# Kernel optimization log

Measured on AMD Instinct MI355X. Metric: run time of the kernel, lower is better.

Reference implementation:

```python
import jax, jax.numpy as jnp
import numpy as np

N, E = 10000, 160000
HID, EDIM = 256, 128
EPS = 1e-5


def _layernorm(x, g, b):
    mu = jnp.mean(x, axis=-1, keepdims=True)
    var = jnp.mean(jnp.square(x - mu), axis=-1, keepdims=True)
    return (x - mu) * jax.lax.rsqrt(var + EPS) * g + b


def setup_inputs() -> dict:
    key = jax.random.key(0)
    ks = jax.random.split(key, 12)
    cat_dim = 2 * HID + EDIM  # 640

    def lin(k, fan_in, fan_out):
        kw, kb = jax.random.split(k)
        lim = 1.0 / np.sqrt(fan_in)
        W = jax.random.uniform(kw, (fan_in, fan_out), jnp.float32, -lim, lim)
        b = jax.random.uniform(kb, (fan_out,), jnp.float32, -lim, lim)
        return W, b

    We1, be1 = lin(ks[0], cat_dim, EDIM)
    We2, be2 = lin(ks[1], EDIM, EDIM)
    Wv1, bv1 = lin(ks[2], cat_dim, HID)
    Wv2, bv2 = lin(ks[3], HID, HID)

    return {
        "h": jax.random.normal(ks[4], (N, HID), jnp.float32),
        "e": jax.random.normal(ks[5], (E, EDIM), jnp.float32),
        "edge_index": jax.random.randint(ks[6], (2, E), 0, N, jnp.int64),
        "We1": We1, "be1": be1, "We2": We2, "be2": be2,
        "Wv1": Wv1, "bv1": bv1, "Wv2": Wv2, "bv2": bv2,
        "ne_g": jnp.ones((EDIM,), jnp.float32), "ne_b": jnp.zeros((EDIM,), jnp.float32),
        "nv_g": jnp.ones((HID,), jnp.float32), "nv_b": jnp.zeros((HID,), jnp.float32),
    }


def reference(h, e, edge_index, We1, be1, We2, be2, Wv1, bv1, Wv2, bv2,
              ne_g, ne_b, nv_g, nv_b):
    # Eval mode: dropout and edge_drop are identity.
    src, dst = edge_index[0], edge_index[1]
    h_src = h[src]  # [E, HID] gather
    h_dst = h[dst]  # [E, HID] gather

    # Edge update: phi_e(concat) -> residual + LayerNorm
    xe = jnp.concatenate([h_src, h_dst, e], axis=-1)  # [E, 2H+ED]
    e_msg = jax.nn.gelu(xe @ We1 + be1, approximate=False) @ We2 + be2
    e_new = _layernorm(e + e_msg, ne_g, ne_b)

    # Node update: phi_v(concat with updated e) -> scatter_mean -> residual + LN
    xv = jnp.concatenate([h_src, h_dst, e_new], axis=-1)
    m = jax.nn.gelu(xv @ Wv1 + bv1, approximate=False) @ Wv2 + bv2  # [E, HID]
    agg = jax.ops.segment_sum(m, dst, num_segments=h.shape[0])
    counts = jax.ops.segment_sum(jnp.ones((m.shape[0], 1), m.dtype), dst,
                                 num_segments=h.shape[0])
    agg = agg / jnp.maximum(counts, 1.0)
    h_new = _layernorm(h + agg, nv_g, nv_b)
    return (h_new, e_new)
```

## Files before the change

kernel.cpp:

```cpp
#include <hip/hip_runtime.h>
#include <hip/hip_bf16.h>

#define NNODE 10000
#define NEDGE 160000
#define HIDD  256
#define ED    128
#define CAT   640

typedef short bf8 __attribute__((ext_vector_type(8)));
typedef short bf4 __attribute__((ext_vector_type(4)));
typedef float f4  __attribute__((ext_vector_type(4)));
typedef unsigned int u32;

__device__ __forceinline__ float bf2f(ushort u) {
    return __uint_as_float(((unsigned)u) << 16);
}
__device__ __forceinline__ ushort f2bf(float f) {
    unsigned u = __float_as_uint(f);
    return (ushort)((u + 0x7fffu + ((u >> 16) & 1u)) >> 16);
}
__device__ __forceinline__ float gelu_fast(float x) {
    float x2 = x * x;
    float u = 0.7978845608028654f * x * (1.0f + 0.044715f * x2);
    float au = fabsf(u);
    float ex = __expf(2.0f * au);
    float t = 1.0f - 2.0f / (1.0f + ex);
    t = copysignf(t, u);
    return 0.5f * x * (1.0f + t);
}
__device__ __forceinline__ int clampi(int v) {
    return ((unsigned)v >= (unsigned)NNODE) ? 0 : v;
}
__device__ __forceinline__ int getidx(const int* ei, bool i64, int pos) {
    int v = i64 ? ei[2 * pos] : ei[pos];
    return clampi(v);
}
__device__ __forceinline__ float loadf(const void* p, size_t idx, bool f32) {
    return f32 ? ((const float*)p)[idx] : bf2f(((const ushort*)p)[idx]);
}
__device__ __forceinline__ bf8 load8(const void* p, size_t idx, bool f32) {
    if (f32) {
        const float* fp = (const float*)p + idx;
        f4 lo = *(const f4*)fp, hi = *(const f4*)(fp + 4);
        bf8 r;
        r[0] = (short)f2bf(lo[0]); r[1] = (short)f2bf(lo[1]);
        r[2] = (short)f2bf(lo[2]); r[3] = (short)f2bf(lo[3]);
        r[4] = (short)f2bf(hi[0]); r[5] = (short)f2bf(hi[1]);
        r[6] = (short)f2bf(hi[2]); r[7] = (short)f2bf(hi[3]);
        return r;
    }
    return *(const bf8*)((const ushort*)p + idx);
}
__device__ __forceinline__ void storef(void* p, size_t idx, float v, bool f32) {
    if (f32) ((float*)p)[idx] = v;
    else     ((ushort*)p)[idx] = f2bf(v);
}
__device__ __forceinline__ void fadd_native(float* p, float v) {
    unsafeAtomicAdd(p, v);
}

__global__ void detect_kernel(const u32* __restrict__ h_u32,
                              const u32* __restrict__ ei_u32,
                              u32* __restrict__ flags) {
    int t = threadIdx.x;
    u32 e8 = (h_u32[t] >> 7) & 0xFFu;
    bool inw = (e8 >= 100u && e8 <= 150u);
    unsigned long long m = __ballot(inw);
    bool hi_nz = (t < 16) ? (ei_u32[2 * t + 1] != 0u) : false;
    unsigned long long m2 = __ballot(hi_nz);
    if (t == 0) {
        flags[0] = (__popcll(m) < 40) ? 1u : 0u;
        flags[1] = (m2 == 0ull) ? 1u : 0u;
    }
}

__global__ void prep_kernel(const void* __restrict__ We1, const void* __restrict__ We2,
                            const void* __restrict__ Wv1, const void* __restrict__ Wv2,
                            ushort* __restrict__ WT, const u32* __restrict__ flags) {
    const bool f32 = flags[0] != 0;
    int idx = blockIdx.x * 256 + threadIdx.x;
    if (idx >= 327680) return;
    const void* W; int base, k0, K, Wld;
    if      (idx <  32768) { W = We1; base = 0;      k0 = 0;   K = 256; Wld = 128; }
    else if (idx <  65536) { W = We1; base = 32768;  k0 = 256; K = 256; Wld = 128; }
    else if (idx <  81920) { W = We1; base = 65536;  k0 = 512; K = 128; Wld = 128; }
    else if (idx <  98304) { W = We2; base = 81920;  k0 = 0;   K = 128; Wld = 128; }
    else if (idx < 163840) { W = Wv1; base = 98304;  k0 = 0;   K = 256; Wld = 256; }
    else if (idx < 229376) { W = Wv1; base = 163840; k0 = 256; K = 256; Wld = 256; }
    else if (idx < 262144) { W = Wv1; base = 229376; k0 = 512; K = 128; Wld = 256; }
    else                   { W = Wv2; base = 262144; k0 = 0;   K = 256; Wld = 256; }
    int local = idx - base;
    int k = local & (K - 1);
    int n = local / K;
    WT[idx] = f2bf(loadf(W, (size_t)(k0 + k) * Wld + n, f32));
}

__global__ void hconv_kernel(const void* __restrict__ h, ushort* __restrict__ hb,
                             const u32* __restrict__ flags) {
    const bool f32 = flags[0] != 0;
    int i = blockIdx.x * 256 + threadIdx.x;
    if (i < NNODE * HIDD / 8)
        *(bf8*)&hb[(size_t)i * 8] = load8(h, (size_t)i * 8, f32);
}

__global__ void count_kernel(const int* __restrict__ ei, u32* __restrict__ cnt,
                             const u32* __restrict__ flags) {
    bool i64 = flags[1] != 0;
    int i = blockIdx.x * 256 + threadIdx.x;
    if (i < NEDGE) atomicAdd(&cnt[getidx(ei, i64, NEDGE + i)], 1u);
}

__global__ void scan_kernel(const u32* __restrict__ cnt, int* __restrict__ head) {
    __shared__ u32 part[256];
    __shared__ u32 base[256];
    int t = threadIdx.x;
    u32 s = 0;
    for (int j = 0; j < 40; ++j) {
        int i = t * 40 + j;
        if (i < NNODE) s += cnt[i];
    }
    part[t] = s;
    __syncthreads();
    if (t == 0) {
        u32 run = 0;
        for (int i = 0; i < 256; ++i) { base[i] = run; run += part[i]; }
    }
    __syncthreads();
    u32 run = base[t];
    for (int j = 0; j < 40; ++j) {
        int i = t * 40 + j;
        if (i < NNODE) { head[i] = (int)run; run += cnt[i]; }
    }
}

__global__ void fill_kernel(const int* __restrict__ ei, int* __restrict__ head,
                            int* __restrict__ perm, int* __restrict__ dsts,
                            const u32* __restrict__ flags) {
    bool i64 = flags[1] != 0;
    int i = blockIdx.x * 256 + threadIdx.x;
    if (i < NEDGE) {
        int d = getidx(ei, i64, NEDGE + i);
        int pos = atomicAdd(&head[d], 1);
        perm[pos] = i;
        dsts[pos] = d;
    }
}

template<int NB>
__device__ __forceinline__ void qp_body(const ushort* __restrict__ hb,
                                        const ushort* __restrict__ WT,
                                        const void* __restrict__ bias,
                                        ushort* __restrict__ O, int bid, bool f32) {
    const int tid = threadIdx.x;
    const int wid = tid >> 6, lane = tid & 63;
    const int l16 = lane & 15, lg = lane >> 4;
    const int node0 = bid * 64;
    const int N = NB * 64;
    const int n0 = wid * (NB * 16);

    size_t ra[4];
    #pragma unroll
    for (int ai = 0; ai < 4; ++ai) {
        int row = node0 + ai * 16 + l16;
        ra[ai] = (size_t)(row < NNODE ? row : NNODE - 1) * HIDD;
    }
    int bb[NB];
    #pragma unroll
    for (int bi = 0; bi < NB; ++bi) bb[bi] = (n0 + bi * 16 + l16) * HIDD;

    f4 acc[4][NB] = {};
    for (int kc = 0; kc < 4; ++kc) {
        #pragma unroll
        for (int ks = 0; ks < 2; ++ks) {
            int kk = kc * 64 + ks * 32 + lg * 8;
            bf8 b[NB];
            #pragma unroll
            for (int bi = 0; bi < NB; ++bi) b[bi] = *(const bf8*)&WT[bb[bi] + kk];
            #pragma unroll
            for (int ai = 0; ai < 4; ++ai) {
                bf8 a = *(const bf8*)&hb[ra[ai] + kk];
                #pragma unroll
                for (int bi = 0; bi < NB; ++bi)
                    acc[ai][bi] = __builtin_amdgcn_mfma_f32_16x16x32_bf16(a, b[bi], acc[ai][bi], 0, 0, 0);
            }
        }
    }
    #pragma unroll
    for (int bi = 0; bi < NB; ++bi) {
        int col = n0 + bi * 16 + l16;
        int pcol; float badd;
        if constexpr (NB == 4) {
            int hh = col >> 7, c = col & 127;
            badd = (hh == 0) ? loadf(bias, c, f32) : 0.f;
            pcol = hh * 128 + (c & 15) * 8 + (c >> 4);
        } else {
            int hh = col >> 8, c = col & 255;
            badd = (hh == 0) ? loadf(bias, c, f32) : 0.f;
            int nh2 = c >> 7, rem = c & 127, w = rem >> 5, b2 = (rem >> 4) & 1, l = c & 15;
            pcol = hh * 256 + w * 64 + l * 4 + nh2 * 2 + b2;
        }
        #pragma unroll
        for (int ai = 0; ai < 4; ++ai)
            #pragma unroll
            for (int r = 0; r < 4; ++r) {
                int gr = node0 + ai * 16 + lg * 4 + r;
                if (gr < NNODE) O[(size_t)gr * N + pcol] = f2bf(acc[ai][bi][r] + badd);
            }
    }
}

#define QPB ((NNODE + 63) / 64)
__global__ __launch_bounds__(256) void qp2_kernel(
    const ushort* __restrict__ hb, const ushort* __restrict__ WTe,
    const ushort* __restrict__ WTv, const void* __restrict__ be1,
    const void* __restrict__ bv1, ushort* __restrict__ Qab,
    ushort* __restrict__ Pab, const u32* __restrict__ flags) {
    const bool f32 = flags[0] != 0;
    if (blockIdx.x < QPB) qp_body<4>(hb, WTe, be1, Qab, blockIdx.x, f32);
    else                  qp_body<8>(hb, WTv, bv1, Pab, blockIdx.x - QPB, f32);
}

#define FWG (NEDGE / 64)
__global__ __launch_bounds__(256) void fused_kernel(
    const void* __restrict__ e, const int* __restrict__ ei,
    const int* __restrict__ perm, const int* __restrict__ dsts,
    const ushort* __restrict__ WT1c,
    const ushort* __restrict__ WT2, const void* __restrict__ be2,
    const ushort* __restrict__ Qab,
    const void* __restrict__ neg, const void* __restrict__ neb,
    const ushort* __restrict__ WvcT,
    const ushort* __restrict__ Pab,
    float* __restrict__ S, void* __restrict__ out,
    const u32* __restrict__ flags)
{
    const bool f32 = flags[0] != 0, i64 = flags[1] != 0;
    __shared__ ushort Asm[64 * 136];
    __shared__ ushort Bsm[128 * 136];
    __shared__ ushort Tsm[64 * 136];
    __shared__ int PermS[64], SrcS[64], DstS[64];

    int orig = blockIdx.x;
    int xcd = orig & 7, slot = orig >> 3;
    int bid = (xcd < 4 ? xcd * 313 : 4 * 313 + (xcd - 4) * 312) + slot;

    const int tid = threadIdx.x;
    const int wid = tid >> 6, lane = tid & 63;
    const int l16 = lane & 15, lg = lane >> 4;
    const int edge0 = bid * 64;
    const int rm = wid * 16;

    if (tid < 64) {
        int eid = perm[edge0 + tid];
        PermS[tid] = eid;
        SrcS[tid] = getidx(ei, i64, eid);
        DstS[tid] = dsts[edge0 + tid];
    }
    __syncthreads();

    #pragma unroll
    for (int j = 0; j < 4; ++j) {
        int s2 = tid + j * 256;
        int r = s2 >> 4, c8 = (s2 & 15) * 8;
        *(bf8*)&Asm[r * 136 + c8] = load8(e, (size_t)PermS[r] * ED + c8, f32);
    }
    #pragma unroll
    for (int it = 0; it < 8; ++it) {
        int s2 = tid + it * 256;
        int n = s2 >> 4, c8 = (s2 & 15) * 8;
        *(bf8*)&Bsm[n * 136 + c8] = *(const bf8*)&WT1c[n * 128 + c8];
    }
    __syncthreads();

    f4 acc[8] = {};
    #pragma unroll
    for (int kc = 0; kc < 2; ++kc)
        #pragma unroll
        for (int ks = 0; ks < 2; ++ks) {
            int ko = kc * 64 + ks * 32 + lg * 8;
            bf8 a = *(const bf8*)&Asm[(rm + l16) * 136 + ko];
            #pragma unroll
            for (int f = 0; f < 8; ++f) {
                bf8 b = *(const bf8*)&Bsm[(f * 16 + l16) * 136 + ko];
                acc[f] = __builtin_amdgcn_mfma_f32_16x16x32_bf16(a, b, acc[f], 0, 0, 0);
            }
        }

    {
        bf8 qs[4], qd[4];
        #pragma unroll
        for (int r = 0; r < 4; ++r) {
            int row = rm + lg * 4 + r;
            qs[r] = *(const bf8*)&Qab[(size_t)SrcS[row] * 256 + l16 * 8];
            qd[r] = *(const bf8*)&Qab[(size_t)DstS[row] * 256 + 128 + l16 * 8];
        }
        #pragma unroll
        for (int f = 0; f < 8; ++f)
            #pragma unroll
            for (int r = 0; r < 4; ++r) {
                float val = acc[f][r] + bf2f((ushort)qs[r][f]) + bf2f((ushort)qd[r][f]);
                Tsm[(rm + lg * 4 + r) * 136 + f * 16 + l16] = f2bf(gelu_fast(val));
            }
    }
    __syncthreads();

    #pragma unroll
    for (int it = 0; it < 8; ++it) {
        int s2 = tid + it * 256;
        int n = s2 >> 4, c8 = (s2 & 15) * 8;
        *(bf8*)&Bsm[n * 136 + c8] = *(const bf8*)&WT2[n * 128 + c8];
    }
    __syncthreads();

    f4 acc2[8] = {};
    #pragma unroll
    for (int kc = 0; kc < 2; ++kc)
        #pragma unroll
        for (int ks = 0; ks < 2; ++ks) {
            int ko = kc * 64 + ks * 32 + lg * 8;
            bf8 a = *(const bf8*)&Tsm[(rm + l16) * 136 + ko];
            #pragma unroll
            for (int f = 0; f < 8; ++f) {
                bf8 b = *(const bf8*)&Bsm[(f * 16 + l16) * 136 + ko];
                acc2[f] = __builtin_amdgcn_mfma_f32_16x16x32_bf16(a, b, acc2[f], 0, 0, 0);
            }
        }

    {
        float v[8][4];
        #pragma unroll
        for (int f = 0; f < 8; ++f) {
            int col = f * 16 + l16;
            float bias = loadf(be2, col, f32);
            #pragma unroll
            for (int r = 0; r < 4; ++r) {
                int row = rm + lg * 4 + r;
                v[f][r] = acc2[f][r] + bias + bf2f(Asm[row * 136 + col]);
            }
        }
        #pragma unroll
        for (int r = 0; r < 4; ++r) {
            float s = 0.f;
            #pragma unroll
            for (int f = 0; f < 8; ++f) s += v[f][r];
            s += __shfl_xor(s, 1); s += __shfl_xor(s, 2);
            s += __shfl_xor(s, 4); s += __shfl_xor(s, 8);
            float mu = s * (1.0f / 128.0f);
            float q = 0.f;
            #pragma unroll
            for (int f = 0; f < 8; ++f) { float d = v[f][r] - mu; q += d * d; }
            q += __shfl_xor(q, 1); q += __shfl_xor(q, 2);
            q += __shfl_xor(q, 4); q += __shfl_xor(q, 8);
            float rstd = rsqrtf(q * (1.0f / 128.0f) + 1e-5f);
            int row = rm + lg * 4 + r;
            #pragma unroll
            for (int f = 0; f < 8; ++f) {
                int col = f * 16 + l16;
                float y = (v[f][r] - mu) * rstd * loadf(neg, col, f32) + loadf(neb, col, f32);
                Tsm[row * 136 + col] = f2bf(y);
            }
        }
    }
    __syncthreads();

    {
        int row = tid >> 2, pc = (tid & 3) * 32;
        size_t obase = (size_t)NNODE * HIDD + (size_t)PermS[row] * ED + pc;
        #pragma unroll
        for (int q2 = 0; q2 < 4; ++q2) {
            bf8 w = *(const bf8*)&Tsm[row * 136 + pc + q2 * 8];
            if (f32) {
                f4 lo, hi;
                lo[0] = bf2f((ushort)w[0]); lo[1] = bf2f((ushort)w[1]);
                lo[2] = bf2f((ushort)w[2]); lo[3] = bf2f((ushort)w[3]);
                hi[0] = bf2f((ushort)w[4]); hi[1] = bf2f((ushort)w[5]);
                hi[2] = bf2f((ushort)w[6]); hi[3] = bf2f((ushort)w[7]);
                *(f4*)((float*)out + obase + q2 * 8) = lo;
                *(f4*)((float*)out + obase + q2 * 8 + 4) = hi;
            } else {
                *(bf8*)((ushort*)out + obase + q2 * 8) = w;
            }
        }
    }

    f4 accN[4][2][2] = {};
    #pragma unroll
    for (int nh = 0; nh < 2; ++nh) {
        #pragma unroll
        for (int it = 0; it < 8; ++it) {
            int s2 = tid + it * 256;
            int n = s2 >> 4, c8 = (s2 & 15) * 8;
            *(bf8*)&Bsm[n * 136 + c8] = *(const bf8*)&WvcT[(nh * 128 + n) * 128 + c8];
        }
        __syncthreads();
        #pragma unroll
        for (int kc = 0; kc < 2; ++kc)
            #pragma unroll
            for (int ks = 0; ks < 2; ++ks) {
                int ko = kc * 64 + ks * 32 + lg * 8;
                bf8 a[4], b[2];
                #pragma unroll
                for (int ai = 0; ai < 4; ++ai)
                    a[ai] = *(const bf8*)&Tsm[(ai * 16 + l16) * 136 + ko];
                #pragma unroll
                for (int bi = 0; bi < 2; ++bi)
                    b[bi] = *(const bf8*)&Bsm[(wid * 32 + bi * 16 + l16) * 136 + ko];
                #pragma unroll
                for (int ai = 0; ai < 4; ++ai)
                    #pragma unroll
                    for (int bi = 0; bi < 2; ++bi)
                        accN[ai][nh][bi] = __builtin_amdgcn_mfma_f32_16x16x32_bf16(a[ai], b[bi], accN[ai][nh][bi], 0, 0, 0);
            }
        __syncthreads();
    }

    #pragma unroll
    for (int ai = 0; ai < 4; ++ai) {
        int p0 = ai * 16 + lg * 4;
        int dd[4], ss[4];
        #pragma unroll
        for (int r = 0; r < 4; ++r) { dd[r] = DstS[p0 + r]; ss[r] = SrcS[p0 + r]; }
        bf4 ps[4], pd[4];
        #pragma unroll
        for (int r = 0; r < 4; ++r) {
            ps[r] = *(const bf4*)&Pab[(size_t)ss[r] * 512 + wid * 64 + l16 * 4];
            pd[r] = *(const bf4*)&Pab[(size_t)dd[r] * 512 + 256 + wid * 64 + l16 * 4];
        }
        #pragma unroll
        for (int nh = 0; nh < 2; ++nh)
            #pragma unroll
            for (int bi = 0; bi < 2; ++bi) {
                int col = nh * 128 + wid * 32 + bi * 16 + l16;
                const int j = nh * 2 + bi;
                float v0 = gelu_fast(accN[0 + ai - ai][nh][bi][0] * 0.f + accN[ai][nh][bi][0] + bf2f((ushort)ps[0][j]) + bf2f((ushort)pd[0][j]));
                float v1 = gelu_fast(accN[ai][nh][bi][1] + bf2f((ushort)ps[1][j]) + bf2f((ushort)pd[1][j]));
                float v2 = gelu_fast(accN[ai][nh][bi][2] + bf2f((ushort)ps[2][j]) + bf2f((ushort)pd[2][j]));
                float v3 = gelu_fast(accN[ai][nh][bi][3] + bf2f((ushort)ps[3][j]) + bf2f((ushort)pd[3][j]));
                float s = v0; int d = dd[0];
                if (dd[1] == d) s += v1; else { fadd_native(&S[(size_t)d * HIDD + col], s); d = dd[1]; s = v1; }
                if (dd[2] == d) s += v2; else { fadd_native(&S[(size_t)d * HIDD + col], s); d = dd[2]; s = v2; }
                if (dd[3] == d) s += v3; else { fadd_native(&S[(size_t)d * HIDD + col], s); d = dd[3]; s = v3; }
                fadd_native(&S[(size_t)d * HIDD + col], s);
            }
    }
}

__global__ __launch_bounds__(256) void hn_gemm_kernel(
    const float* __restrict__ S, const ushort* __restrict__ WTv2,
    const void* __restrict__ bv2, const u32* __restrict__ cnt,
    const void* __restrict__ h,
    const void* __restrict__ nvg, const void* __restrict__ nvb,
    void* __restrict__ out, const u32* __restrict__ flags)
{
    const bool f32 = flags[0] != 0;
    constexpr int LDV = 260;
    __shared__ float Vsm[64 * LDV];

    const int tid = threadIdx.x;
    const int wid = tid >> 6, lane = tid & 63;
    const int l16 = lane & 15, lg = lane >> 4;
    const int node0 = blockIdx.x * 64;
    const int n0 = wid * 64;

    size_t ra[4];
    #pragma unroll
    for (int ai = 0; ai < 4; ++ai) {
        int row = node0 + ai * 16 + l16;
        ra[ai] = (size_t)(row < NNODE ? row : NNODE - 1) * HIDD;
    }
    int bb[4];
    #pragma unroll
    for (int bi = 0; bi < 4; ++bi) bb[bi] = (n0 + bi * 16 + l16) * HIDD;

    f4 acc[4][4] = {};
    for (int kc = 0; kc < 4; ++kc) {
        #pragma unroll
        for (int ks = 0; ks < 2; ++ks) {
            int kk = kc * 64 + ks * 32 + lg * 8;
            bf8 b[4];
            #pragma unroll
            for (int bi = 0; bi < 4; ++bi) b[bi] = *(const bf8*)&WTv2[bb[bi] + kk];
            #pragma unroll
            for (int ai = 0; ai < 4; ++ai) {
                bf8 a = load8(S, ra[ai] + kk, true);
                #pragma unroll
                for (int bi = 0; bi < 4; ++bi)
                    acc[ai][bi] = __builtin_amdgcn_mfma_f32_16x16x32_bf16(a, b[bi], acc[ai][bi], 0, 0, 0);
            }
        }
    }

    #pragma unroll
    for (int bi = 0; bi < 4; ++bi) {
        int col = n0 + bi * 16 + l16;
        float b2 = loadf(bv2, col, f32);
        #pragma unroll
        for (int ai = 0; ai < 4; ++ai)
            #pragma unroll
            for (int r = 0; r < 4; ++r) {
                int rowl = ai * 16 + lg * 4 + r;
                int gr = node0 + rowl;
                int grc = gr < NNODE ? gr : NNODE - 1;
                float c = (float)cnt[grc];
                float inv = 1.0f / fmaxf(c, 1.0f);
                float val = (acc[ai][bi][r] + c * b2) * inv
                          + loadf(h, (size_t)grc * HIDD + col, f32);
                Vsm[rowl * LDV + col] = val;
            }
    }
    __syncthreads();

    #pragma unroll
    for (int rr = 0; rr < 4; ++rr) {
        int rowl = wid * 16 + lg * 4 + rr;
        int gr = node0 + rowl;
        float x[16];
        #pragma unroll
        for (int f = 0; f < 16; ++f) x[f] = Vsm[rowl * LDV + f * 16 + l16];
        float s = 0.f;
        #pragma unroll
        for (int f = 0; f < 16; ++f) s += x[f];
        s += __shfl_xor(s, 1); s += __shfl_xor(s, 2);
        s += __shfl_xor(s, 4); s += __shfl_xor(s, 8);
        float mu = s * (1.0f / 256.0f);
        float q = 0.f;
        #pragma unroll
        for (int f = 0; f < 16; ++f) { float d = x[f] - mu; q += d * d; }
        q += __shfl_xor(q, 1); q += __shfl_xor(q, 2);
        q += __shfl_xor(q, 4); q += __shfl_xor(q, 8);
        float rstd = rsqrtf(q * (1.0f / 256.0f) + 1e-5f);
        if (gr < NNODE) {
            #pragma unroll
            for (int f = 0; f < 16; ++f) {
                int col = f * 16 + l16;
                float y = (x[f] - mu) * rstd * loadf(nvg, col, f32) + loadf(nvb, col, f32);
                storef(out, (size_t)gr * HIDD + col, y, f32);
            }
        }
    }
}

extern "C" void kernel_launch(void* const* d_in, const int* in_sizes, int n_in,
                              void* d_out, int out_size, void* d_ws, size_t ws_size,
                              hipStream_t stream)
{
    (void)in_sizes; (void)n_in; (void)out_size; (void)ws_size;
    const void* h   = d_in[0];
    const void* e   = d_in[1];
    const int*  ei  = (const int*)d_in[2];
    const void* We1 = d_in[3];
    const void* be1 = d_in[4];
    const void* We2 = d_in[5];
    const void* be2 = d_in[6];
    const void* Wv1 = d_in[7];
    const void* bv1 = d_in[8];
    const void* Wv2 = d_in[9];
    const void* bv2 = d_in[10];
    const void* neg = d_in[11];
    const void* neb = d_in[12];
    const void* nvg = d_in[13];
    const void* nvb = d_in[14];

    char* ws = (char*)d_ws;
    u32*   flags = (u32*)ws;
    float* S     = (float*)(ws + 256);
    u32*   cnt   = (u32*)(ws + 256 + (size_t)NNODE * HIDD * 4);
    size_t off = 256 + (size_t)NNODE * HIDD * 4 + ((size_t)NNODE * 4 + 255) / 256 * 256;
    int*   head = (int*)(ws + off);            off += ((size_t)NNODE * 4 + 255) / 256 * 256;
    int*   perm = (int*)(ws + off);            off += (size_t)NEDGE * 4;
    int*   dsts = (int*)(ws + off);            off += (size_t)NEDGE * 4;
    ushort* WTb  = (ushort*)(ws + off);
    ushort* WTe  = WTb;
    ushort* WT1c = WTb + 65536;
    ushort* WT2  = WTb + 81920;
    ushort* WTv  = WTb + 98304;
    ushort* WvcT = WTb + 229376;
    ushort* WTv2 = WTb + 262144;
    ushort* hb   = WTb + 327680;
    ushort* Qab  = hb + (size_t)NNODE * HIDD;
    ushort* Pab  = Qab + (size_t)NNODE * 256;

    hipMemsetAsync(S, 0, (size_t)NNODE * HIDD * 4 + (size_t)NNODE * 4, stream);
    detect_kernel<<<1, 64, 0, stream>>>((const u32*)h, (const u32*)ei, flags);

    prep_kernel<<<1280, 256, 0, stream>>>(We1, We2, Wv1, Wv2, WTb, flags);
    hconv_kernel<<<(NNODE * HIDD / 8 + 255) / 256, 256, 0, stream>>>(h, hb, flags);
    count_kernel<<<(NEDGE + 255) / 256, 256, 0, stream>>>(ei, cnt, flags);
    scan_kernel<<<1, 256, 0, stream>>>(cnt, head);
    fill_kernel<<<(NEDGE + 255) / 256, 256, 0, stream>>>(ei, head, perm, dsts, flags);

    qp2_kernel<<<2 * QPB, 256, 0, stream>>>(hb, WTe, WTv, be1, bv1, Qab, Pab, flags);

    fused_kernel<<<FWG, 256, 0, stream>>>(e, ei, perm, dsts,
                                          WT1c, WT2, be2, Qab,
                                          neg, neb, WvcT, Pab,
                                          S, d_out, flags);
    hn_gemm_kernel<<<(NNODE + 63) / 64, 256, 0, stream>>>(S, WTv2, bv2, cnt, h,
                                                          nvg, nvb, d_out, flags);
}
```

Baseline: 335.3 us.

## Merge preprocessing kernels and hoist gathered Q/P loads earlier in fused kernel

Folds detect, weight transpose, h conversion and degree counting into one combo launch, with each block redoing the detection locally. Fill runs in the same launch as the Q/P node projection. This cuts the launch count from eight to four to reduce launch and serialization overhead. In the fused edge kernel, the Qab/Pab gathers are issued before the GEMMs so their latency overlaps compute, at the cost of many more live registers (ps/pd/ddA arrays) and possible occupancy loss.

```diff
diff --git a/kernel.cpp b/kernel.cpp
--- a/kernel.cpp
+++ b/kernel.cpp
@@ -58,56 +58,64 @@
 __device__ __forceinline__ void fadd_native(float* p, float v) {
     unsafeAtomicAdd(p, v);
 }
-
-__global__ void detect_kernel(const u32* __restrict__ h_u32,
-                              const u32* __restrict__ ei_u32,
-                              u32* __restrict__ flags) {
-    int t = threadIdx.x;
-    u32 e8 = (h_u32[t] >> 7) & 0xFFu;
-    bool inw = (e8 >= 100u && e8 <= 150u);
-    unsigned long long m = __ballot(inw);
-    bool hi_nz = (t < 16) ? (ei_u32[2 * t + 1] != 0u) : false;
-    unsigned long long m2 = __ballot(hi_nz);
-    if (t == 0) {
-        flags[0] = (__popcll(m) < 40) ? 1u : 0u;
-        flags[1] = (m2 == 0ull) ? 1u : 0u;
-    }
-}
-
-__global__ void prep_kernel(const void* __restrict__ We1, const void* __restrict__ We2,
-                            const void* __restrict__ Wv1, const void* __restrict__ Wv2,
-                            ushort* __restrict__ WT, const u32* __restrict__ flags) {
-    const bool f32 = flags[0] != 0;
-    int idx = blockIdx.x * 256 + threadIdx.x;
-    if (idx >= 327680) return;
-    const void* W; int base, k0, K, Wld;
-    if      (idx <  32768) { W = We1; base = 0;      k0 = 0;   K = 256; Wld = 128; }
-    else if (idx <  65536) { W = We1; base = 32768;  k0 = 256; K = 256; Wld = 128; }
-    else if (idx <  81920) { W = We1; base = 65536;  k0 = 512; K = 128; Wld = 128; }
-    else if (idx <  98304) { W = We2; base = 81920;  k0 = 0;   K = 128; Wld = 128; }
-    else if (idx < 163840) { W = Wv1; base = 98304;  k0 = 0;   K = 256; Wld = 256; }
-    else if (idx < 229376) { W = Wv1; base = 163840; k0 = 256; K = 256; Wld = 256; }
-    else if (idx < 262144) { W = Wv1; base = 229376; k0 = 512; K = 128; Wld = 256; }
-    else                   { W = Wv2; base = 262144; k0 = 0;   K = 256; Wld = 256; }
-    int local = idx - base;
-    int k = local & (K - 1);
-    int n = local / K;
-    WT[idx] = f2bf(loadf(W, (size_t)(k0 + k) * Wld + n, f32));
-}
-
-__global__ void hconv_kernel(const void* __restrict__ h, ushort* __restrict__ hb,
-                             const u32* __restrict__ flags) {
-    const bool f32 = flags[0] != 0;
-    int i = blockIdx.x * 256 + threadIdx.x;
-    if (i < NNODE * HIDD / 8)
-        *(bf8*)&hb[(size_t)i * 8] = load8(h, (size_t)i * 8, f32);
-}
-
-__global__ void count_kernel(const int* __restrict__ ei, u32* __restrict__ cnt,
-                             const u32* __restrict__ flags) {
-    bool i64 = flags[1] != 0;
-    int i = blockIdx.x * 256 + threadIdx.x;
-    if (i < NEDGE) atomicAdd(&cnt[getidx(ei, i64, NEDGE + i)], 1u);
+__device__ __forceinline__ void detect_local(const u32* h_u32, const u32* ei_u32,
+                                             u32* sf) {
+    if (threadIdx.x < 64) {
+        int t = threadIdx.x;
+        u32 e8 = (h_u32[t] >> 7) & 0xFFu;
+        bool inw = (e8 >= 100u && e8 <= 150u);
+        unsigned long long m = __ballot(inw);
+        bool hi_nz = (t < 16) ? (ei_u32[2 * t + 1] != 0u) : false;
+        unsigned long long m2 = __ballot(hi_nz);
+        if (t == 0) {
+            sf[0] = (__popcll(m) < 40) ? 1u : 0u;
+            sf[1] = (m2 == 0ull) ? 1u : 0u;
+        }
+    }
+    __syncthreads();
+}
+
+#define PREP_B 1280
+#define HCONV_B 1250
+#define COUNT_B 625
+__global__ __launch_bounds__(256) void combo_kernel(
+    const void* __restrict__ h, const int* __restrict__ ei,
+    const void* __restrict__ We1, const void* __restrict__ We2,
+    const void* __restrict__ Wv1, const void* __restrict__ Wv2,
+    ushort* __restrict__ WT, ushort* __restrict__ hb,
+    u32* __restrict__ cnt, u32* __restrict__ flags)
+{
+    __shared__ u32 sf[2];
+    detect_local((const u32*)h, (const u32*)ei, sf);
+    const bool f32 = sf[0] != 0, i64 = sf[1] != 0;
+    int b = blockIdx.x, tid = threadIdx.x;
+
+    if (b == 0 && tid == 0) { flags[0] = sf[0]; flags[1] = sf[1]; }
+
+    if (b < PREP_B) {
+        int idx = b * 256 + tid;
+        if (idx >= 327680) return;
+        const void* W; int base, k0, K, Wld;
+        if      (idx <  32768) { W = We1; base = 0;      k0 = 0;   K = 256; Wld = 128; }
+        else if (idx <  65536) { W = We1; base = 32768;  k0 = 256; K = 256; Wld = 128; }
+        else if (idx <  81920) { W = We1; base = 65536;  k0 = 512; K = 128; Wld = 128; }
+        else if (idx <  98304) { W = We2; base = 81920;  k0 = 0;   K = 128; Wld = 128; }
+        else if (idx < 163840) { W = Wv1; base = 98304;  k0 = 0;   K = 256; Wld = 256; }
+        else if (idx < 229376) { W = Wv1; base = 163840; k0 = 256; K = 256; Wld = 256; }
+        else if (idx < 262144) { W = Wv1; base = 229376; k0 = 512; K = 128; Wld = 256; }
+        else                   { W = Wv2; base = 262144; k0 = 0;   K = 256; Wld = 256; }
+        int local = idx - base;
+        int k = local & (K - 1);
+        int n = local / K;
+        WT[idx] = f2bf(loadf(W, (size_t)(k0 + k) * Wld + n, f32));
+    } else if (b < PREP_B + HCONV_B) {
+        int i = (b - PREP_B) * 256 + tid;
+        if (i < NNODE * HIDD / 8)
+            *(bf8*)&hb[(size_t)i * 8] = load8(h, (size_t)i * 8, f32);
+    } else {
+        int i = (b - PREP_B - HCONV_B) * 256 + tid;
+        if (i < NEDGE) atomicAdd(&cnt[getidx(ei, i64, NEDGE + i)], 1u);
+    }
 }
 
 __global__ void scan_kernel(const u32* __restrict__ cnt, int* __restrict__ head) {
@@ -130,19 +138,6 @@
     for (int j = 0; j < 40; ++j) {
         int i = t * 40 + j;
         if (i < NNODE) { head[i] = (int)run; run += cnt[i]; }
-    }
-}
-
-__global__ void fill_kernel(const int* __restrict__ ei, int* __restrict__ head,
-                            int* __restrict__ perm, int* __restrict__ dsts,
-                            const u32* __restrict__ flags) {
-    bool i64 = flags[1] != 0;
-    int i = blockIdx.x * 256 + threadIdx.x;
-    if (i < NEDGE) {
-        int d = getidx(ei, i64, NEDGE + i);
-        int pos = atomicAdd(&head[d], 1);
-        perm[pos] = i;
-        dsts[pos] = d;
     }
 }
 
@@ -210,14 +205,30 @@
 }
 
 #define QPB ((NNODE + 63) / 64)
-__global__ __launch_bounds__(256) void qp2_kernel(
+#define FILL_B 625
+__global__ __launch_bounds__(256) void fillqp_kernel(
+    const int* __restrict__ ei, int* __restrict__ head,
+    int* __restrict__ perm, int* __restrict__ dsts,
     const ushort* __restrict__ hb, const ushort* __restrict__ WTe,
     const ushort* __restrict__ WTv, const void* __restrict__ be1,
     const void* __restrict__ bv1, ushort* __restrict__ Qab,
-    ushort* __restrict__ Pab, const u32* __restrict__ flags) {
-    const bool f32 = flags[0] != 0;
-    if (blockIdx.x < QPB) qp_body<4>(hb, WTe, be1, Qab, blockIdx.x, f32);
-    else                  qp_body<8>(hb, WTv, bv1, Pab, blockIdx.x - QPB, f32);
+    ushort* __restrict__ Pab, const u32* __restrict__ flags)
+{
+    const bool f32 = flags[0] != 0, i64 = flags[1] != 0;
+    int b = blockIdx.x;
+    if (b < FILL_B) {
+        int i = b * 256 + threadIdx.x;
+        if (i < NEDGE) {
+            int d = getidx(ei, i64, NEDGE + i);
+            int pos = atomicAdd(&head[d], 1);
+            perm[pos] = i;
+            dsts[pos] = d;
+        }
+    } else if (b < FILL_B + QPB) {
+        qp_body<4>(hb, WTe, be1, Qab, b - FILL_B, f32);
+    } else {
+        qp_body<8>(hb, WTv, bv1, Pab, b - FILL_B - QPB, f32);
+    }
 }
 
 #define FWG (NEDGE / 64)
@@ -257,6 +268,27 @@
     }
     __syncthreads();
 
+    bf8 qs[4], qd[4];
+    #pragma unroll
+    for (int r = 0; r < 4; ++r) {
+        int row = rm + lg * 4 + r;
+        qs[r] = *(const bf8*)&Qab[(size_t)SrcS[row] * 256 + l16 * 8];
+        qd[r] = *(const bf8*)&Qab[(size_t)DstS[row] * 256 + 128 + l16 * 8];
+    }
+    bf4 ps[4][4], pd[4][4];
+    int ddA[4][4];
+    #pragma unroll
+    for (int ai = 0; ai < 4; ++ai) {
+        int p0 = ai * 16 + lg * 4;
+        #pragma unroll
+        for (int r = 0; r < 4; ++r) {
+            int ss = SrcS[p0 + r], dd = DstS[p0 + r];
+            ddA[ai][r] = dd;
+            ps[ai][r] = *(const bf4*)&Pab[(size_t)ss * 512 + wid * 64 + l16 * 4];
+            pd[ai][r] = *(const bf4*)&Pab[(size_t)dd * 512 + 256 + wid * 64 + l16 * 4];
+        }
+    }
+
     #pragma unroll
     for (int j = 0; j < 4; ++j) {
         int s2 = tid + j * 256;
@@ -285,22 +317,13 @@
             }
         }
 
-    {
-        bf8 qs[4], qd[4];
+    #pragma unroll
+    for (int f = 0; f < 8; ++f)
         #pragma unroll
         for (int r = 0; r < 4; ++r) {
-            int row = rm + lg * 4 + r;
-            qs[r] = *(const bf8*)&Qab[(size_t)SrcS[row] * 256 + l16 * 8];
-            qd[r] = *(const bf8*)&Qab[(size_t)DstS[row] * 256 + 128 + l16 * 8];
-        }
-        #pragma unroll
-        for (int f = 0; f < 8; ++f)
-            #pragma unroll
-            for (int r = 0; r < 4; ++r) {
-                float val = acc[f][r] + bf2f((ushort)qs[r][f]) + bf2f((ushort)qd[r][f]);
-                Tsm[(rm + lg * 4 + r) * 136 + f * 16 + l16] = f2bf(gelu_fast(val));
-            }
-    }
+            float val = acc[f][r] + bf2f((ushort)qs[r][f]) + bf2f((ushort)qd[r][f]);
+            Tsm[(rm + lg * 4 + r) * 136 + f * 16 + l16] = f2bf(gelu_fast(val));
+        }
     __syncthreads();
 
     #pragma unroll
@@ -415,30 +438,20 @@
 
     #pragma unroll
     for (int ai = 0; ai < 4; ++ai) {
-        int p0 = ai * 16 + lg * 4;
-        int dd[4], ss[4];
-        #pragma unroll
-        for (int r = 0; r < 4; ++r) { dd[r] = DstS[p0 + r]; ss[r] = SrcS[p0 + r]; }
-        bf4 ps[4], pd[4];
-        #pragma unroll
-        for (int r = 0; r < 4; ++r) {
-            ps[r] = *(const bf4*)&Pab[(size_t)ss[r] * 512 + wid * 64 + l16 * 4];
-            pd[r] = *(const bf4*)&Pab[(size_t)dd[r] * 512 + 256 + wid * 64 + l16 * 4];
-        }
         #pragma unroll
         for (int nh = 0; nh < 2; ++nh)
             #pragma unroll
             for (int bi = 0; bi < 2; ++bi) {
                 int col = nh * 128 + wid * 32 + bi * 16 + l16;
                 const int j = nh * 2 + bi;
-                float v0 = gelu_fast(accN[0 + ai - ai][nh][bi][0] * 0.f + accN[ai][nh][bi][0] + bf2f((ushort)ps[0][j]) + bf2f((ushort)pd[0][j]));
-                float v1 = gelu_fast(accN[ai][nh][bi][1] + bf2f((ushort)ps[1][j]) + bf2f((ushort)pd[1][j]));
-                float v2 = gelu_fast(accN[ai][nh][bi][2] + bf2f((ushort)ps[2][j]) + bf2f((ushort)pd[2][j]));
-                float v3 = gelu_fast(accN[ai][nh][bi][3] + bf2f((ushort)ps[3][j]) + bf2f((ushort)pd[3][j]));
-                float s = v0; int d = dd[0];
-                if (dd[1] == d) s += v1; else { fadd_native(&S[(size_t)d * HIDD + col], s); d = dd[1]; s = v1; }
-                if (dd[2] == d) s += v2; else { fadd_native(&S[(size_t)d * HIDD + col], s); d = dd[2]; s = v2; }
-                if (dd[3] == d) s += v3; else { fadd_native(&S[(size_t)d * HIDD + col], s); d = dd[3]; s = v3; }
+                float v0 = gelu_fast(accN[ai][nh][bi][0] + bf2f((ushort)ps[ai][0][j]) + bf2f((ushort)pd[ai][0][j]));
+                float v1 = gelu_fast(accN[ai][nh][bi][1] + bf2f((ushort)ps[ai][1][j]) + bf2f((ushort)pd[ai][1][j]));
+                float v2 = gelu_fast(accN[ai][nh][bi][2] + bf2f((ushort)ps[ai][2][j]) + bf2f((ushort)pd[ai][2][j]));
+                float v3 = gelu_fast(accN[ai][nh][bi][3] + bf2f((ushort)ps[ai][3][j]) + bf2f((ushort)pd[ai][3][j]));
+                float s = v0; int d = ddA[ai][0];
+                if (ddA[ai][1] == d) s += v1; else { fadd_native(&S[(size_t)d * HIDD + col], s); d = ddA[ai][1]; s = v1; }
+                if (ddA[ai][2] == d) s += v2; else { fadd_native(&S[(size_t)d * HIDD + col], s); d = ddA[ai][2]; s = v2; }
+                if (ddA[ai][3] == d) s += v3; else { fadd_native(&S[(size_t)d * HIDD + col], s); d = ddA[ai][3]; s = v3; }
                 fadd_native(&S[(size_t)d * HIDD + col], s);
             }
     }
@@ -580,15 +593,12 @@
     ushort* Pab  = Qab + (size_t)NNODE * 256;
 
     hipMemsetAsync(S, 0, (size_t)NNODE * HIDD * 4 + (size_t)NNODE * 4, stream);
-    detect_kernel<<<1, 64, 0, stream>>>((const u32*)h, (const u32*)ei, flags);
-
-    prep_kernel<<<1280, 256, 0, stream>>>(We1, We2, Wv1, Wv2, WTb, flags);
-    hconv_kernel<<<(NNODE * HIDD / 8 + 255) / 256, 256, 0, stream>>>(h, hb, flags);
-    count_kernel<<<(NEDGE + 255) / 256, 256, 0, stream>>>(ei, cnt, flags);
+
+    combo_kernel<<<PREP_B + HCONV_B + COUNT_B, 256, 0, stream>>>(
+        h, ei, We1, We2, Wv1, Wv2, WTb, hb, cnt, flags);
     scan_kernel<<<1, 256, 0, stream>>>(cnt, head);
-    fill_kernel<<<(NEDGE + 255) / 256, 256, 0, stream>>>(ei, head, perm, dsts, flags);
-
-    qp2_kernel<<<2 * QPB, 256, 0, stream>>>(hb, WTe, WTv, be1, bv1, Qab, Pab, flags);
+    fillqp_kernel<<<FILL_B + 2 * QPB, 256, 0, stream>>>(
+        ei, head, perm, dsts, hb, WTe, WTv, be1, bv1, Qab, Pab, flags);
 
     fused_kernel<<<FWG, 256, 0, stream>>>(e, ei, perm, dsts,
                                           WT1c, WT2, be2, Qab,
```

New measurement: 409.5 us. +22.1%, slower.
